# Kernel tuning notes

Hardware: AMD Instinct MI355X
Metric: run time of the kernel (lower is better)

## Reference

```python
import jax, jax.numpy as jnp
import numpy as np

LAMBDA = 0.01  # sparsity_threshold
SCALE = 0.02
NUM_BLOCKS = 4


def setup_inputs() -> dict:
    key = jax.random.key(0)
    k1, k2, k3, k4, k5 = jax.random.split(key, 5)
    B, N, C = 8, 4096, 512
    bs = C // NUM_BLOCKS
    return {
        "x": jax.random.normal(k1, (B, N, C), dtype=jnp.float32),
        "w1": jax.random.normal(k2, (2, NUM_BLOCKS, bs, bs), dtype=jnp.float32) * SCALE,
        "w2": jax.random.normal(k3, (2, NUM_BLOCKS, bs, bs), dtype=jnp.float32) * SCALE,
        "b1": jax.random.normal(k4, (2, NUM_BLOCKS, bs), dtype=jnp.float32) * SCALE,
        "b2": jax.random.normal(k5, (2, NUM_BLOCKS, bs), dtype=jnp.float32) * SCALE,
        "H": 64,
        "W": 64,
    }


def _softshrink(v):
    return jnp.where(v > LAMBDA, v - LAMBDA, jnp.where(v < -LAMBDA, v + LAMBDA, jnp.zeros((), v.dtype)))


def reference(x, w1, w2, b1, b2, H, W):
    B, N, C = x.shape
    bs = C // NUM_BLOCKS
    xb = x.reshape(B, N, NUM_BLOCKS, bs)
    # FFT over (token, block) axes, ortho norm — faithful to torch fft2(dim=(1,2))
    xf = jnp.fft.fft2(xb, axes=(1, 2), norm="ortho")
    re, im = jnp.real(xf), jnp.imag(xf)

    mul = lambda a, w: jnp.einsum("tnbd,bdk->tnbk", a, w)  # block-diagonal matmul

    r1 = jax.nn.relu(mul(re, w1[0]) - mul(im, w1[1]) + b1[0])
    i1 = jax.nn.relu(mul(re, w1[1]) + mul(im, w1[0]) + b1[1])
    r2 = mul(r1, w2[0]) - mul(i1, w2[1]) + b2[0]
    i2 = mul(r1, w2[1]) + mul(i1, w2[0]) + b2[1]

    z = _softshrink(r2) + 1j * _softshrink(i2)
    out = jnp.real(jnp.fft.ifft2(z, axes=(1, 2), norm="ortho"))  # .to(float32) keeps real part
    return out.reshape(B, N, C).astype(jnp.float32)
```

## Files before the change

kernel.cpp:

```cpp
#include <hip/hip_runtime.h>
#include <math.h>

#define TWO_PI 6.283185307179586f

typedef __attribute__((ext_vector_type(8))) short bf16x8;
typedef __attribute__((ext_vector_type(4))) short bf16x4;
typedef __attribute__((ext_vector_type(4))) float f32x4;
typedef __attribute__((ext_vector_type(4))) _Float16 h16x4;
typedef __attribute__((ext_vector_type(8))) _Float16 h16x8;

__device__ __forceinline__ short f2bf(float f) {
    unsigned u = __float_as_uint(f);
    unsigned r = (u + 0x7FFFu + ((u >> 16) & 1u)) >> 16;
    return (short)r;
}
__device__ __forceinline__ float bf2f(short s) {
    return __uint_as_float(((unsigned)(unsigned short)s) << 16);
}

__device__ __forceinline__ int dr4(int s) {
    return ((s & 3) << 4) | (s & 12) | ((s >> 4) & 3);
}

__device__ __forceinline__ void cmulw(float& xr, float& xi, float wr, float wi) {
    const float tr = xr * wr - xi * wi;
    xi = xr * wi + xi * wr;
    xr = tr;
}

__device__ __forceinline__ f32x4 ld4bf(const char* Z, int off) {
    const bf16x4 v = *(const bf16x4*)(Z + off);
    f32x4 r;
    r[0] = bf2f(v[0]); r[1] = bf2f(v[1]); r[2] = bf2f(v[2]); r[3] = bf2f(v[3]);
    return r;
}
__device__ __forceinline__ void st4bf(char* Z, int off, f32x4 a) {
    bf16x4 v;
    v[0] = f2bf(a[0]); v[1] = f2bf(a[1]); v[2] = f2bf(a[2]); v[3] = f2bf(a[3]);
    *(bf16x4*)(Z + off) = v;
}

__device__ __forceinline__ int swzoff(int r, int cb) {
    return r * 256 + (cb ^ ((r & 7) << 4));
}

__device__ __forceinline__ void dif_stage_bf(char* Z, const float* wtr, const float* wti,
                                             int cb, int h, int s) {
    const int q  = 16 >> (2 * s);
    const int tw = 1 << (2 * s);
    const int j = h & (q - 1);
    const int g = (s == 0) ? 0 : (h >> (4 - 2 * s));
    const int i0 = g * (q << 2) + j;
    const int i1 = i0 + q, i2 = i1 + q, i3 = i2 + q;
    const int o0 = swzoff(i0, cb), o1 = swzoff(i1, cb);
    const int o2 = swzoff(i2, cb), o3 = swzoff(i3, cb);
    const f32x4 a0r = ld4bf(Z, o0), a0i = ld4bf(Z + 16384, o0);
    const f32x4 a1r = ld4bf(Z, o1), a1i = ld4bf(Z + 16384, o1);
    const f32x4 a2r = ld4bf(Z, o2), a2i = ld4bf(Z + 16384, o2);
    const f32x4 a3r = ld4bf(Z, o3), a3i = ld4bf(Z + 16384, o3);
    const int m = j * tw;
    const float w1r = wtr[m],     w1i = wti[m];
    const float w2r = wtr[2 * m], w2i = wti[2 * m];
    const float w3r = wtr[3 * m], w3i = wti[3 * m];
    f32x4 O0r, O0i, O1r, O1i, O2r, O2i, O3r, O3i;
#pragma unroll
    for (int e = 0; e < 4; ++e) {
        const float t0r = a0r[e] + a2r[e], t0i = a0i[e] + a2i[e];
        const float t2r = a0r[e] - a2r[e], t2i = a0i[e] - a2i[e];
        const float t1r = a1r[e] + a3r[e], t1i = a1i[e] + a3i[e];
        const float dr  = a1r[e] - a3r[e], di  = a1i[e] - a3i[e];
        const float t3r = di, t3i = -dr;
        O0r[e] = t0r + t1r;  O0i[e] = t0i + t1i;
        float y1r = t2r + t3r, y1i = t2i + t3i;
        float y2r = t0r - t1r, y2i = t0i - t1i;
        float y3r = t2r - t3r, y3i = t2i - t3i;
        if (m) {
            cmulw(y1r, y1i, w1r, w1i);
            cmulw(y2r, y2i, w2r, w2i);
            cmulw(y3r, y3i, w3r, w3i);
        }
        O1r[e] = y1r; O1i[e] = y1i;
        O2r[e] = y2r; O2i[e] = y2i;
        O3r[e] = y3r; O3i[e] = y3i;
    }
    st4bf(Z, o0, O0r);  st4bf(Z + 16384, o0, O0i);
    st4bf(Z, o1, O1r);  st4bf(Z + 16384, o1, O1i);
    st4bf(Z, o2, O2r);  st4bf(Z + 16384, o2, O2i);
    st4bf(Z, o3, O3r);  st4bf(Z + 16384, o3, O3i);
}

__device__ __forceinline__ void dit_stage_bf(char* Z, const float* wtr, const float* wti,
                                             int cb, int h, int s) {
    const int q  = 16 >> (2 * s);
    const int tw = 1 << (2 * s);
    const int j = h & (q - 1);
    const int g = (s == 0) ? 0 : (h >> (4 - 2 * s));
    const int i0 = g * (q << 2) + j;
    const int i1 = i0 + q, i2 = i1 + q, i3 = i2 + q;
    const int o0 = swzoff(i0, cb), o1 = swzoff(i1, cb);
    const int o2 = swzoff(i2, cb), o3 = swzoff(i3, cb);
    const f32x4 a0r = ld4bf(Z, o0), a0i = ld4bf(Z + 16384, o0);
    const f32x4 a1r = ld4bf(Z, o1), a1i = ld4bf(Z + 16384, o1);
    const f32x4 a2r = ld4bf(Z, o2), a2i = ld4bf(Z + 16384, o2);
    const f32x4 a3r = ld4bf(Z, o3), a3i = ld4bf(Z + 16384, o3);
    const int m = j * tw;
    const float w1r = wtr[m],     w1i = -wti[m];
    const float w2r = wtr[2 * m], w2i = -wti[2 * m];
    const float w3r = wtr[3 * m], w3i = -wti[3 * m];
    f32x4 O0r, O0i, O1r, O1i, O2r, O2i, O3r, O3i;
#pragma unroll
    for (int e = 0; e < 4; ++e) {
        float b1r = a1r[e], b1i = a1i[e];
        float b2r = a2r[e], b2i = a2i[e];
        float b3r = a3r[e], b3i = a3i[e];
        if (m) {
            cmulw(b1r, b1i, w1r, w1i);
            cmulw(b2r, b2i, w2r, w2i);
            cmulw(b3r, b3i, w3r, w3i);
        }
        const float u0r = a0r[e] + b2r, u0i = a0i[e] + b2i;
        const float u1r = a0r[e] - b2r, u1i = a0i[e] - b2i;
        const float u2r = b1r + b3r,    u2i = b1i + b3i;
        const float dr  = b1r - b3r,    di  = b1i - b3i;
        const float u3r = -di, u3i = dr;
        O0r[e] = u0r + u2r; O0i[e] = u0i + u2i;
        O1r[e] = u1r + u3r; O1i[e] = u1i + u3i;
        O2r[e] = u0r - u2r; O2i[e] = u0i - u2i;
        O3r[e] = u1r - u3r; O3i[e] = u1i - u3i;
    }
    st4bf(Z, o0, O0r);  st4bf(Z + 16384, o0, O0i);
    st4bf(Z, o1, O1r);  st4bf(Z + 16384, o1, O1i);
    st4bf(Z, o2, O2r);  st4bf(Z + 16384, o2, O2i);
    st4bf(Z, o3, O3r);  st4bf(Z + 16384, o3, O3i);
}

__device__ __forceinline__ void stage_ztile(const short* __restrict__ zre,
                                            const short* __restrict__ zim,
                                            char* Zbuf, int b, int dg, int ct,
                                            int wave, int lane) {
#pragma unroll
    for (int it = 0; it < 4; ++it) {
        const int q = wave * 256 + it * 64 + lane;
        const int p = q >> 10;
        const int r = q & 1023;
        const int slot = r >> 4;
        const int c = r & 15;
        const int c_log = c ^ (slot & 7);
        const int blk = c_log >> 2, cj = c_log & 3;
        const short* src = p ? zim : zre;
        const size_t g = ((size_t)(b * 4096 + dg * 64 + slot) * 512)
                       + (size_t)(blk * 128 + ct * 32 + cj * 8);
        unsigned* lp = (unsigned*)(Zbuf + (wave * 4096 + it * 1024));
        __builtin_amdgcn_global_load_lds((const unsigned*)(src + g), lp, 16, 0, 0);
    }
}

#define DECODE_BCT() \
    const int b  = blockIdx.x >> 8; \
    const int dg = (blockIdx.x >> 2) & 63; \
    const int ct = blockIdx.x & 3;

#define GADDR(slot, blk, f4) \
    (((size_t)(b * 4096 + (slot)) * 512) + (size_t)((blk) * 128 + ct * 32 + (f4) * 4))

#define SETUP_TABLE48() \
    if (tid < 48) { \
        float s_, c_; \
        sincosf(TWO_PI * (float)tid / 64.0f, &s_, &c_); \
        wre[tid] = c_; wim[tid] = -s_; \
    }

template<int W>
__device__ __forceinline__ void fft64_dif4v(_Float16 (*Lre)[W], _Float16 (*Lim)[W],
                                            const float* wtr, const float* wti,
                                            int c4, int h) {
#pragma unroll
    for (int s = 0; s < 3; ++s) {
        const int q  = 16 >> (2 * s);
        const int tw = 1 << (2 * s);
        __syncthreads();
        const int j = h & (q - 1);
        const int g = (s == 0) ? 0 : (h >> (4 - 2 * s));
        const int i0 = g * (q << 2) + j;
        const int i1 = i0 + q, i2 = i1 + q, i3 = i2 + q;
        const h16x4 A0r = *(const h16x4*)&Lre[i0][c4], A0i = *(const h16x4*)&Lim[i0][c4];
        const h16x4 A1r = *(const h16x4*)&Lre[i1][c4], A1i = *(const h16x4*)&Lim[i1][c4];
        const h16x4 A2r = *(const h16x4*)&Lre[i2][c4], A2i = *(const h16x4*)&Lim[i2][c4];
        const h16x4 A3r = *(const h16x4*)&Lre[i3][c4], A3i = *(const h16x4*)&Lim[i3][c4];
        const int m = j * tw;
        const float w1r = wtr[m],     w1i = wti[m];
        const float w2r = wtr[2 * m], w2i = wti[2 * m];
        const float w3r = wtr[3 * m], w3i = wti[3 * m];
        h16x4 O0r, O0i, O1r, O1i, O2r, O2i, O3r, O3i;
#pragma unroll
        for (int e = 0; e < 4; ++e) {
            const float a0r = (float)A0r[e], a0i = (float)A0i[e];
            const float a1r = (float)A1r[e], a1i = (float)A1i[e];
            const float a2r = (float)A2r[e], a2i = (float)A2i[e];
            const float a3r = (float)A3r[e], a3i = (float)A3i[e];
            const float t0r = a0r + a2r, t0i = a0i + a2i;
            const float t2r = a0r - a2r, t2i = a0i - a2i;
            const float t1r = a1r + a3r, t1i = a1i + a3i;
            const float dr  = a1r - a3r, di  = a1i - a3i;
            const float t3r = di, t3i = -dr;
            O0r[e] = (_Float16)(t0r + t1r);  O0i[e] = (_Float16)(t0i + t1i);
            float y1r = t2r + t3r, y1i = t2i + t3i;
            float y2r = t0r - t1r, y2i = t0i - t1i;
            float y3r = t2r - t3r, y3i = t2i - t3i;
            if (m) {
                cmulw(y1r, y1i, w1r, w1i);
                cmulw(y2r, y2i, w2r, w2i);
                cmulw(y3r, y3i, w3r, w3i);
            }
            O1r[e] = (_Float16)y1r; O1i[e] = (_Float16)y1i;
            O2r[e] = (_Float16)y2r; O2i[e] = (_Float16)y2i;
            O3r[e] = (_Float16)y3r; O3i[e] = (_Float16)y3i;
        }
        *(h16x4*)&Lre[i0][c4] = O0r;  *(h16x4*)&Lim[i0][c4] = O0i;
        *(h16x4*)&Lre[i1][c4] = O1r;  *(h16x4*)&Lim[i1][c4] = O1i;
        *(h16x4*)&Lre[i2][c4] = O2r;  *(h16x4*)&Lim[i2][c4] = O2i;
        *(h16x4*)&Lre[i3][c4] = O3r;  *(h16x4*)&Lim[i3][c4] = O3i;
    }
    __syncthreads();
}

template<int W>
__device__ __forceinline__ void fft64_dit4v(_Float16 (*Lre)[W], _Float16 (*Lim)[W],
                                            const float* wtr, const float* wti,
                                            int c4, int h) {
#pragma unroll
    for (int s = 2; s >= 0; --s) {
        const int q  = 16 >> (2 * s);
        const int tw = 1 << (2 * s);
        __syncthreads();
        const int j = h & (q - 1);
        const int g = (s == 0) ? 0 : (h >> (4 - 2 * s));
        const int i0 = g * (q << 2) + j;
        const int i1 = i0 + q, i2 = i1 + q, i3 = i2 + q;
        const h16x4 A0r = *(const h16x4*)&Lre[i0][c4], A0i = *(const h16x4*)&Lim[i0][c4];
        const h16x4 A1r = *(const h16x4*)&Lre[i1][c4], A1i = *(const h16x4*)&Lim[i1][c4];
        const h16x4 A2r = *(const h16x4*)&Lre[i2][c4], A2i = *(const h16x4*)&Lim[i2][c4];
        const h16x4 A3r = *(const h16x4*)&Lre[i3][c4], A3i = *(const h16x4*)&Lim[i3][c4];
        const int m = j * tw;
        const float w1r = wtr[m],     w1i = -wti[m];
        const float w2r = wtr[2 * m], w2i = -wti[2 * m];
        const float w3r = wtr[3 * m], w3i = -wti[3 * m];
        h16x4 O0r, O0i, O1r, O1i, O2r, O2i, O3r, O3i;
#pragma unroll
        for (int e = 0; e < 4; ++e) {
            float b1r = (float)A1r[e], b1i = (float)A1i[e];
            float b2r = (float)A2r[e], b2i = (float)A2i[e];
            float b3r = (float)A3r[e], b3i = (float)A3i[e];
            if (m) {
                cmulw(b1r, b1i, w1r, w1i);
                cmulw(b2r, b2i, w2r, w2i);
                cmulw(b3r, b3i, w3r, w3i);
            }
            const float a0r = (float)A0r[e], a0i = (float)A0i[e];
            const float u0r = a0r + b2r, u0i = a0i + b2i;
            const float u1r = a0r - b2r, u1i = a0i - b2i;
            const float u2r = b1r + b3r, u2i = b1i + b3i;
            const float dr  = b1r - b3r, di  = b1i - b3i;
            const float u3r = -di, u3i = dr;
            O0r[e] = (_Float16)(u0r + u2r); O0i[e] = (_Float16)(u0i + u2i);
            O1r[e] = (_Float16)(u1r + u3r); O1i[e] = (_Float16)(u1i + u3i);
            O2r[e] = (_Float16)(u0r - u2r); O2i[e] = (_Float16)(u0i - u2i);
            O3r[e] = (_Float16)(u1r - u3r); O3i[e] = (_Float16)(u1i - u3i);
        }
        *(h16x4*)&Lre[i0][c4] = O0r;  *(h16x4*)&Lim[i0][c4] = O0i;
        *(h16x4*)&Lre[i1][c4] = O1r;  *(h16x4*)&Lim[i1][c4] = O1i;
        *(h16x4*)&Lre[i2][c4] = O2r;  *(h16x4*)&Lim[i2][c4] = O2i;
        *(h16x4*)&Lre[i3][c4] = O3r;  *(h16x4*)&Lim[i3][c4] = O3i;
    }
    __syncthreads();
}

extern "C" __global__ void __launch_bounds__(512)
fft_fwd_a(const float* __restrict__ x, short* __restrict__ zre, short* __restrict__ zim) {
    __shared__ __align__(16) _Float16 Lre[64][136];
    __shared__ __align__(16) _Float16 Lim[64][136];
    __shared__ float wre[48], wim[48];
    __shared__ float twr[64], twi[64];
    const int tid = threadIdx.x;
    SETUP_TABLE48();
    DECODE_BCT();
    if (tid >= 64 && tid < 128) {
        const int s1 = tid - 64;
        float sn, cs;
        sincosf(-(TWO_PI / 4096.0f) * (float)(dg * dr4(s1)), &sn, &cs);
        twr[s1] = cs; twi[s1] = sn;
    }
    for (int idx = tid; idx < 2048; idx += 512) {
        const int n1 = idx >> 5, q = idx & 31, blk = q >> 3, f4 = q & 7;
        const int cl = blk * 32 + f4 * 4;
        const float4 v = *(const float4*)(x + GADDR(n1 * 64 + dg, blk, f4));
        h16x4 hv, hz;
        hv[0] = (_Float16)v.x; hv[1] = (_Float16)v.y;
        hv[2] = (_Float16)v.z; hv[3] = (_Float16)v.w;
        hz[0] = (_Float16)0.f; hz[1] = (_Float16)0.f;
        hz[2] = (_Float16)0.f; hz[3] = (_Float16)0.f;
        *(h16x4*)&Lre[n1][cl] = hv;
        *(h16x4*)&Lim[n1][cl] = hz;
    }
    fft64_dif4v<136>(Lre, Lim, wre, wim, (tid & 31) * 4, tid >> 5);
    {
        const int s1 = tid >> 3, f4 = tid & 7;
        const float cs = twr[s1], sn = twi[s1];
        f32x4 r[4], m[4];
#pragma unroll
        for (int blk = 0; blk < 4; ++blk) {
            const int cl = blk * 32 + f4 * 4;
            const h16x4 hr = *(const h16x4*)&Lre[s1][cl];
            const h16x4 hi = *(const h16x4*)&Lim[s1][cl];
#pragma unroll
            for (int e = 0; e < 4; ++e) {
                const float vr = (float)hr[e], vi = (float)hi[e];
                r[blk][e] = vr * cs - vi * sn;
                m[blk][e] = vr * sn + vi * cs;
            }
        }
        const float sc = 1.0f / 128.0f;
        f32x4 yr[4], ym[4];
#pragma unroll
        for (int e = 0; e < 4; ++e) {
            const float r0 = r[0][e], r1 = r[1][e], r2 = r[2][e], r3 = r[3][e];
            const float m0 = m[0][e], m1 = m[1][e], m2 = m[2][e], m3 = m[3][e];
            yr[0][e] = (r0 + r1 + r2 + r3) * sc;  ym[0][e] = (m0 + m1 + m2 + m3) * sc;
            yr[1][e] = (r0 + m1 - r2 - m3) * sc;  ym[1][e] = (m0 - r1 - m2 + r3) * sc;
            yr[2][e] = (r0 - r1 + r2 - r3) * sc;  ym[2][e] = (m0 - m1 + m2 - m3) * sc;
            yr[3][e] = (r0 - m1 - r2 + m3) * sc;  ym[3][e] = (m0 + r1 - m2 - r3) * sc;
        }
#pragma unroll
        for (int blk = 0; blk < 4; ++blk) {
            bf16x4 pr, pi;
#pragma unroll
            for (int e = 0; e < 4; ++e) {
                pr[e] = f2bf(yr[blk][e]);
                pi[e] = f2bf(ym[blk][e]);
            }
            const size_t g = GADDR(s1 * 64 + dg, blk, f4);
            *(bf16x4*)(zre + g) = pr;
            *(bf16x4*)(zim + g) = pi;
        }
    }
}

extern "C" __global__ void __launch_bounds__(512)
fft_fwd_b(short* __restrict__ zre, short* __restrict__ zim) {
    __shared__ __align__(16) char Zs[32768];
    __shared__ float wre[48], wim[48];
    const int tid = threadIdx.x;
    SETUP_TABLE48();
    const int bh = blockIdx.x >> 8;
    const int dg = (blockIdx.x >> 2) & 63;
    const int ct = blockIdx.x & 3;
    const int wave = tid >> 6, lane = tid & 63;
    const int cb = (tid & 31) * 8;
    const int h  = tid >> 5;

    stage_ztile(zre, zim, Zs, bh * 2, dg, ct, wave, lane);

    for (int t = 0; t < 2; ++t) {
        __syncthreads();
        dif_stage_bf(Zs, wre, wim, cb, h, 0);
        __syncthreads();
        dif_stage_bf(Zs, wre, wim, cb, h, 1);
        __syncthreads();
        dif_stage_bf(Zs, wre, wim, cb, h, 2);
        __syncthreads();
        bf16x8 vout[4];
#pragma unroll
        for (int kq = 0; kq < 4; ++kq) {
            const int q = wave * 256 + kq * 64 + lane;
            vout[kq] = *(const bf16x8*)(Zs + q * 16);
        }
        __syncthreads();
        if (t + 1 < 2)
            stage_ztile(zre, zim, Zs, bh * 2 + t + 1, dg, ct, wave, lane);
        const int b = bh * 2 + t;
#pragma unroll
        for (int kq = 0; kq < 4; ++kq) {
            const int q = wave * 256 + kq * 64 + lane;
            const int p = q >> 10;
            const int r2 = q & 1023;
            const int slot = r2 >> 4;
            const int c = r2 & 15;
            const int c_log = c ^ (slot & 7);
            const int blk = c_log >> 2, cj = c_log & 3;
            short* dst = p ? zim : zre;
            const size_t g = ((size_t)(b * 4096 + dg * 64 + slot) * 512)
                           + (size_t)(blk * 128 + ct * 32 + cj * 8);
            *(bf16x8*)(dst + g) = vout[kq];
        }
    }
}

extern "C" __global__ void __launch_bounds__(512)
fft_inv_a(short* __restrict__ zre, short* __restrict__ zim) {
    __shared__ __align__(16) char Zs[32768];
    __shared__ float wre[48], wim[48];
    __shared__ float twr[64], twi[64];
    const int tid = threadIdx.x;
    SETUP_TABLE48();
    const int bh = blockIdx.x >> 8;
    const int dg = (blockIdx.x >> 2) & 63;
    const int ct = blockIdx.x & 3;
    if (tid >= 64 && tid < 128) {
        const int n2 = tid - 64;
        float sn, cs;
        sincosf((TWO_PI / 4096.0f) * (float)(n2 * dr4(dg)), &sn, &cs);
        twr[n2] = cs; twi[n2] = sn;
    }
    const int wave = tid >> 6, lane = tid & 63;
    const int cb = (tid & 31) * 8;
    const int h  = tid >> 5;

    stage_ztile(zre, zim, Zs, bh * 2, dg, ct, wave, lane);

    for (int t = 0; t < 2; ++t) {
        __syncthreads();
        dit_stage_bf(Zs, wre, wim, cb, h, 2);
        __syncthreads();
        dit_stage_bf(Zs, wre, wim, cb, h, 1);
        __syncthreads();
        dit_stage_bf(Zs, wre, wim, cb, h, 0);
        __syncthreads();
        bf16x8 pr[2], pi[2];
#pragma unroll
        for (int k = 0; k < 2; ++k) {
            const int idx = tid + k * 512;
            const int slot = idx >> 4;
            const int c = idx & 15;
            const bf16x8 vr = *(const bf16x8*)(Zs + slot * 256 + c * 16);
            const bf16x8 vi = *(const bf16x8*)(Zs + 16384 + slot * 256 + c * 16);
            const float cs = twr[slot], sn = twi[slot];
#pragma unroll
            for (int i = 0; i < 8; ++i) {
                const float ar = bf2f(vr[i]), ai = bf2f(vi[i]);
                pr[k][i] = f2bf(ar * cs - ai * sn);
                pi[k][i] = f2bf(ar * sn + ai * cs);
            }
        }
        __syncthreads();
        if (t + 1 < 2)
            stage_ztile(zre, zim, Zs, bh * 2 + t + 1, dg, ct, wave, lane);
        const int b = bh * 2 + t;
#pragma unroll
        for (int k = 0; k < 2; ++k) {
            const int idx = tid + k * 512;
            const int slot = idx >> 4;
            const int c = idx & 15;
            const int c_log = c ^ (slot & 7);
            const int blk = c_log >> 2, cj = c_log & 3;
            const size_t g = ((size_t)(b * 4096 + dg * 64 + slot) * 512)
                           + (size_t)(blk * 128 + ct * 32 + cj * 8);
            *(bf16x8*)(zre + g) = pr[k];
            *(bf16x8*)(zim + g) = pi[k];
        }
    }
}

extern "C" __global__ void __launch_bounds__(512)
fft_inv_b(const short* __restrict__ zre, const short* __restrict__ zim,
          float* __restrict__ out) {
    __shared__ __align__(16) _Float16 Lre[64][136];
    __shared__ __align__(16) _Float16 Lim[64][136];
    __shared__ float wre[48], wim[48];
    const int tid = threadIdx.x;
    SETUP_TABLE48();
    DECODE_BCT();
    {
        const int s1 = tid >> 3, f4 = tid & 7;
        f32x4 r[4], m[4];
#pragma unroll
        for (int blk = 0; blk < 4; ++blk) {
            const size_t g = GADDR(s1 * 64 + dg, blk, f4);
            const bf16x4 vr = *(const bf16x4*)(zre + g);
            const bf16x4 vi = *(const bf16x4*)(zim + g);
#pragma unroll
            for (int e = 0; e < 4; ++e) {
                r[blk][e] = bf2f(vr[e]);
                m[blk][e] = bf2f(vi[e]);
            }
        }
        const float sc = 1.0f / 128.0f;
        f32x4 yr[4], ym[4];
#pragma unroll
        for (int e = 0; e < 4; ++e) {
            const float r0 = r[0][e], r1 = r[1][e], r2 = r[2][e], r3 = r[3][e];
            const float m0 = m[0][e], m1 = m[1][e], m2 = m[2][e], m3 = m[3][e];
            yr[0][e] = (r0 + r1 + r2 + r3) * sc;  ym[0][e] = (m0 + m1 + m2 + m3) * sc;
            yr[1][e] = (r0 - m1 - r2 + m3) * sc;  ym[1][e] = (m0 + r1 - m2 - r3) * sc;
            yr[2][e] = (r0 - r1 + r2 - r3) * sc;  ym[2][e] = (m0 - m1 + m2 - m3) * sc;
            yr[3][e] = (r0 + m1 - r2 - m3) * sc;  ym[3][e] = (m0 - r1 - m2 + r3) * sc;
        }
#pragma unroll
        for (int blk = 0; blk < 4; ++blk) {
            const int cl = blk * 32 + f4 * 4;
            h16x4 hr, hi;
#pragma unroll
            for (int e = 0; e < 4; ++e) {
                hr[e] = (_Float16)yr[blk][e];
                hi[e] = (_Float16)ym[blk][e];
            }
            *(h16x4*)&Lre[s1][cl] = hr;
            *(h16x4*)&Lim[s1][cl] = hi;
        }
    }
    fft64_dit4v<136>(Lre, Lim, wre, wim, (tid & 31) * 4, tid >> 5);
    for (int idx = tid; idx < 2048; idx += 512) {
        const int n1 = idx >> 5, q = idx & 31, blk = q >> 3, f4 = q & 7;
        const int cl = blk * 32 + f4 * 4;
        const h16x4 hr = *(const h16x4*)&Lre[n1][cl];
        float4 o;
        o.x = (float)hr[0]; o.y = (float)hr[1];
        o.z = (float)hr[2]; o.w = (float)hr[3];
        *(float4*)(out + GADDR(n1 * 64 + dg, blk, f4)) = o;
    }
}

extern "C" __global__ void __launch_bounds__(256)
wprep(const float* __restrict__ w1, const float* __restrict__ w2,
      short* __restrict__ wb) {
    const int i4  = blockIdx.x * 256 + threadIdx.x;
    const int k0  = (i4 & 63) * 4;
    const int n   = (i4 >> 6) & 255;
    const int blk = (i4 >> 14) & 3;
    const int L   = i4 >> 16;
    const float* w = L ? w2 : w1;
    bf16x4 pv;
#pragma unroll
    for (int j = 0; j < 4; ++j) {
        const int k = k0 + j;
        float v;
        if (k < 128) {
            v = (n < 128) ? w[blk * 16384 + k * 128 + n]
                          : w[65536 + blk * 16384 + k * 128 + (n - 128)];
        } else {
            v = (n < 128) ? -w[65536 + blk * 16384 + (k - 128) * 128 + n]
                          :  w[blk * 16384 + (k - 128) * 128 + (n - 128)];
        }
        pv[j] = f2bf(v);
    }
    *(bf16x4*)(wb + (size_t)i4 * 4) = pv;
}

#define MITER 4

__device__ __forceinline__ void stage_tile(const short* __restrict__ zre,
                                           const short* __restrict__ zim,
                                           char* Abuf, int rowbase, int blk,
                                           int wave, int lane) {
#pragma unroll
    for (int it = 0; it < 4; ++it) {
        const int chunk = wave * 256 + it * 64 + lane;
        const int row   = chunk >> 5;
        const unsigned kbyte = ((unsigned)((chunk & 31) << 4)) ^ ((unsigned)((row & 7) << 4));
        const int k0 = (int)(kbyte >> 1);
        const short* src = (k0 < 128) ? zre : zim;
        const size_t g = (size_t)(rowbase + row) * 512 + blk * 128 + (k0 & 127);
        unsigned* lp = (unsigned*)(Abuf + (wave * 4096 + it * 1024));
        __builtin_amdgcn_global_load_lds((const unsigned*)(src + g), lp, 16, 0, 0);
    }
}

template<int LAYER>
__global__ void __launch_bounds__(512)
mlp_mfma(short* __restrict__ zre, short* __restrict__ zim,
         const short* __restrict__ wb, const float* __restrict__ bias) {
    __shared__ __align__(16) char As[2][64 * 256 * 2];

    const int blk  = blockIdx.y;
    const int tid  = threadIdx.x;
    const int wave = tid >> 6;
    const int lane = tid & 63;
    const int lrow = lane & 15;
    const int lk   = lane >> 4;

    bf16x8 Bf[2][8];
#pragma unroll
    for (int nt = 0; nt < 2; ++nt) {
        const int n = wave * 32 + nt * 16 + lrow;
#pragma unroll
        for (int ks = 0; ks < 8; ++ks) {
            Bf[nt][ks] = *(const bf16x8*)(wb + ((size_t)(blk * 256 + n) * 256 + ks * 32 + lk * 8));
        }
    }

    float bv[2];
#pragma unroll
    for (int nt = 0; nt < 2; ++nt) {
        const int n = wave * 32 + nt * 16 + lrow;
        bv[nt] = (n < 128) ? bias[blk * 128 + n] : bias[512 + blk * 128 + (n - 128)];
    }

    stage_tile(zre, zim, As[0], blockIdx.x * MITER * 64, blk, wave, lane);

    for (int t = 0; t < MITER; ++t) {
        __syncthreads();

        if (t + 1 < MITER)
            stage_tile(zre, zim, As[(t + 1) & 1],
                       (blockIdx.x * MITER + t + 1) * 64, blk, wave, lane);

        const char* Ab = As[t & 1];
        const int rowbase = (blockIdx.x * MITER + t) * 64;

        f32x4 acc[4][2];
#pragma unroll
        for (int mt = 0; mt < 4; ++mt)
#pragma unroll
            for (int nt = 0; nt < 2; ++nt)
                acc[mt][nt] = (f32x4){0.f, 0.f, 0.f, 0.f};

#pragma unroll
        for (int ks = 0; ks < 8; ++ks) {
            bf16x8 af[4];
#pragma unroll
            for (int mt = 0; mt < 4; ++mt) {
                const int row = mt * 16 + lrow;
                const int k0  = ks * 32 + lk * 8;
                const unsigned byteoff =
                    ((unsigned)(row * 512 + k0 * 2)) ^ ((unsigned)((row & 7) << 4));
                af[mt] = *(const bf16x8*)(Ab + byteoff);
            }
#pragma unroll
            for (int mt = 0; mt < 4; ++mt)
#pragma unroll
                for (int nt = 0; nt < 2; ++nt)
                    acc[mt][nt] = __builtin_amdgcn_mfma_f32_16x16x32_bf16(
                        af[mt], Bf[nt][ks], acc[mt][nt], 0, 0, 0);
        }

#pragma unroll
        for (int nt = 0; nt < 2; ++nt) {
            const int n = wave * 32 + nt * 16 + lrow;
            short* dst = (n < 128) ? zre : zim;
            const int col = blk * 128 + (n & 127);
#pragma unroll
            for (int mt = 0; mt < 4; ++mt) {
#pragma unroll
                for (int r = 0; r < 4; ++r) {
                    const int row = rowbase + mt * 16 + lk * 4 + r;
                    float v = acc[mt][nt][r] + bv[nt];
                    if (LAYER == 1) {
                        v = fmaxf(v, 0.0f);
                    } else {
                        v = (v > 0.01f) ? v - 0.01f : ((v < -0.01f) ? v + 0.01f : 0.0f);
                    }
                    dst[(size_t)row * 512 + col] = f2bf(v);
                }
            }
        }
    }
}

extern "C" void kernel_launch(void* const* d_in, const int* in_sizes, int n_in,
                              void* d_out, int out_size, void* d_ws, size_t ws_size,
                              hipStream_t stream) {
    const float* x  = (const float*)d_in[0];
    const float* w1 = (const float*)d_in[1];
    const float* w2 = (const float*)d_in[2];
    const float* b1 = (const float*)d_in[3];
    const float* b2 = (const float*)d_in[4];

    float* out = (float*)d_out;
    short* zre = (short*)d_ws;
    short* zim = zre + 16777216;
    short* wb  = (short*)d_out;
    const size_t WB_L = 4ull * 256 * 256;

    wprep<<<512, 256, 0, stream>>>(w1, w2, wb);

    fft_fwd_a<<<2048, 512, 0, stream>>>(x, zre, zim);
    fft_fwd_b<<<1024, 512, 0, stream>>>(zre, zim);

    mlp_mfma<1><<<dim3(32768 / (64 * MITER), 4), 512, 0, stream>>>(zre, zim, wb, b1);
    mlp_mfma<2><<<dim3(32768 / (64 * MITER), 4), 512, 0, stream>>>(zre, zim, wb + WB_L, b2);

    fft_inv_a<<<1024, 512, 0, stream>>>(zre, zim);
    fft_inv_b<<<2048, 512, 0, stream>>>(zre, zim, out);
}
```

Measured before the change: 222.5 us.

## Fuse second FFT stage passes into the MLP matmul kernels

Removes the separate fft_fwd_b and fft_inv_a kernels. Their radix-4 64-point passes now run on the shared-memory A tile inside the layer-1 MLP kernel before the matmul. In the layer-2 kernel, the inverse passes plus the twiddle multiply run on the tile after the softshrink epilogue. This saves two full global read/write round trips of the bf16 spectrum and two launches. In exchange the MLP kernels take extra barriers, per-element sincos calls and FFT arithmetic that delay the MFMA work and the prefetch issue.

```diff
diff --git a/kernel.cpp b/kernel.cpp
--- a/kernel.cpp
+++ b/kernel.cpp
@@ -40,24 +40,38 @@
     *(bf16x4*)(Z + off) = v;
 }
 
-__device__ __forceinline__ int swzoff(int r, int cb) {
-    return r * 256 + (cb ^ ((r & 7) << 4));
-}
-
-__device__ __forceinline__ void dif_stage_bf(char* Z, const float* wtr, const float* wti,
-                                             int cb, int h, int s) {
+#define DECODE_BCT() \
+    const int b  = blockIdx.x >> 8; \
+    const int dg = (blockIdx.x >> 2) & 63; \
+    const int ct = blockIdx.x & 3;
+
+#define GADDR(slot, blk, f4) \
+    (((size_t)(b * 4096 + (slot)) * 512) + (size_t)((blk) * 128 + ct * 32 + (f4) * 4))
+
+#define SETUP_TABLE48() \
+    if (tid < 48) { \
+        float s_, c_; \
+        sincosf(TWO_PI * (float)tid / 64.0f, &s_, &c_); \
+        wre[tid] = c_; wim[tid] = -s_; \
+    }
+
+__device__ __forceinline__ void dif_stage_A(char* Z, const float* wtr, const float* wti,
+                                            int cg, int h, int s) {
     const int q  = 16 >> (2 * s);
     const int tw = 1 << (2 * s);
     const int j = h & (q - 1);
     const int g = (s == 0) ? 0 : (h >> (4 - 2 * s));
     const int i0 = g * (q << 2) + j;
     const int i1 = i0 + q, i2 = i1 + q, i3 = i2 + q;
-    const int o0 = swzoff(i0, cb), o1 = swzoff(i1, cb);
-    const int o2 = swzoff(i2, cb), o3 = swzoff(i3, cb);
-    const f32x4 a0r = ld4bf(Z, o0), a0i = ld4bf(Z + 16384, o0);
-    const f32x4 a1r = ld4bf(Z, o1), a1i = ld4bf(Z + 16384, o1);
-    const f32x4 a2r = ld4bf(Z, o2), a2i = ld4bf(Z + 16384, o2);
-    const f32x4 a3r = ld4bf(Z, o3), a3i = ld4bf(Z + 16384, o3);
+    const int cbR = cg * 8, cbI = cbR + 256;
+    const int oR0 = i0 * 512 + (cbR ^ ((i0 & 7) << 4)), oI0 = i0 * 512 + (cbI ^ ((i0 & 7) << 4));
+    const int oR1 = i1 * 512 + (cbR ^ ((i1 & 7) << 4)), oI1 = i1 * 512 + (cbI ^ ((i1 & 7) << 4));
+    const int oR2 = i2 * 512 + (cbR ^ ((i2 & 7) << 4)), oI2 = i2 * 512 + (cbI ^ ((i2 & 7) << 4));
+    const int oR3 = i3 * 512 + (cbR ^ ((i3 & 7) << 4)), oI3 = i3 * 512 + (cbI ^ ((i3 & 7) << 4));
+    const f32x4 a0r = ld4bf(Z, oR0), a0i = ld4bf(Z, oI0);
+    const f32x4 a1r = ld4bf(Z, oR1), a1i = ld4bf(Z, oI1);
+    const f32x4 a2r = ld4bf(Z, oR2), a2i = ld4bf(Z, oI2);
+    const f32x4 a3r = ld4bf(Z, oR3), a3i = ld4bf(Z, oI3);
     const int m = j * tw;
     const float w1r = wtr[m],     w1i = wti[m];
     const float w2r = wtr[2 * m], w2i = wti[2 * m];
@@ -83,26 +97,29 @@
         O2r[e] = y2r; O2i[e] = y2i;
         O3r[e] = y3r; O3i[e] = y3i;
     }
-    st4bf(Z, o0, O0r);  st4bf(Z + 16384, o0, O0i);
-    st4bf(Z, o1, O1r);  st4bf(Z + 16384, o1, O1i);
-    st4bf(Z, o2, O2r);  st4bf(Z + 16384, o2, O2i);
-    st4bf(Z, o3, O3r);  st4bf(Z + 16384, o3, O3i);
-}
-
-__device__ __forceinline__ void dit_stage_bf(char* Z, const float* wtr, const float* wti,
-                                             int cb, int h, int s) {
+    st4bf(Z, oR0, O0r);  st4bf(Z, oI0, O0i);
+    st4bf(Z, oR1, O1r);  st4bf(Z, oI1, O1i);
+    st4bf(Z, oR2, O2r);  st4bf(Z, oI2, O2i);
+    st4bf(Z, oR3, O3r);  st4bf(Z, oI3, O3i);
+}
+
+__device__ __forceinline__ void dit_stage_A(char* Z, const float* wtr, const float* wti,
+                                            int cg, int h, int s) {
     const int q  = 16 >> (2 * s);
     const int tw = 1 << (2 * s);
     const int j = h & (q - 1);
     const int g = (s == 0) ? 0 : (h >> (4 - 2 * s));
     const int i0 = g * (q << 2) + j;
     const int i1 = i0 + q, i2 = i1 + q, i3 = i2 + q;
-    const int o0 = swzoff(i0, cb), o1 = swzoff(i1, cb);
-    const int o2 = swzoff(i2, cb), o3 = swzoff(i3, cb);
-    const f32x4 a0r = ld4bf(Z, o0), a0i = ld4bf(Z + 16384, o0);
-    const f32x4 a1r = ld4bf(Z, o1), a1i = ld4bf(Z + 16384, o1);
-    const f32x4 a2r = ld4bf(Z, o2), a2i = ld4bf(Z + 16384, o2);
-    const f32x4 a3r = ld4bf(Z, o3), a3i = ld4bf(Z + 16384, o3);
+    const int cbR = cg * 8, cbI = cbR + 256;
+    const int oR0 = i0 * 512 + (cbR ^ ((i0 & 7) << 4)), oI0 = i0 * 512 + (cbI ^ ((i0 & 7) << 4));
+    const int oR1 = i1 * 512 + (cbR ^ ((i1 & 7) << 4)), oI1 = i1 * 512 + (cbI ^ ((i1 & 7) << 4));
+    const int oR2 = i2 * 512 + (cbR ^ ((i2 & 7) << 4)), oI2 = i2 * 512 + (cbI ^ ((i2 & 7) << 4));
+    const int oR3 = i3 * 512 + (cbR ^ ((i3 & 7) << 4)), oI3 = i3 * 512 + (cbI ^ ((i3 & 7) << 4));
+    const f32x4 a0r = ld4bf(Z, oR0), a0i = ld4bf(Z, oI0);
+    const f32x4 a1r = ld4bf(Z, oR1), a1i = ld4bf(Z, oI1);
+    const f32x4 a2r = ld4bf(Z, oR2), a2i = ld4bf(Z, oI2);
+    const f32x4 a3r = ld4bf(Z, oR3), a3i = ld4bf(Z, oI3);
     const int m = j * tw;
     const float w1r = wtr[m],     w1i = -wti[m];
     const float w2r = wtr[2 * m], w2i = -wti[2 * m];
@@ -128,47 +145,11 @@
         O2r[e] = u0r - u2r; O2i[e] = u0i - u2i;
         O3r[e] = u1r - u3r; O3i[e] = u1i - u3i;
     }
-    st4bf(Z, o0, O0r);  st4bf(Z + 16384, o0, O0i);
-    st4bf(Z, o1, O1r);  st4bf(Z + 16384, o1, O1i);
-    st4bf(Z, o2, O2r);  st4bf(Z + 16384, o2, O2i);
-    st4bf(Z, o3, O3r);  st4bf(Z + 16384, o3, O3i);
-}
-
-__device__ __forceinline__ void stage_ztile(const short* __restrict__ zre,
-                                            const short* __restrict__ zim,
-                                            char* Zbuf, int b, int dg, int ct,
-                                            int wave, int lane) {
-#pragma unroll
-    for (int it = 0; it < 4; ++it) {
-        const int q = wave * 256 + it * 64 + lane;
-        const int p = q >> 10;
-        const int r = q & 1023;
-        const int slot = r >> 4;
-        const int c = r & 15;
-        const int c_log = c ^ (slot & 7);
-        const int blk = c_log >> 2, cj = c_log & 3;
-        const short* src = p ? zim : zre;
-        const size_t g = ((size_t)(b * 4096 + dg * 64 + slot) * 512)
-                       + (size_t)(blk * 128 + ct * 32 + cj * 8);
-        unsigned* lp = (unsigned*)(Zbuf + (wave * 4096 + it * 1024));
-        __builtin_amdgcn_global_load_lds((const unsigned*)(src + g), lp, 16, 0, 0);
-    }
-}
-
-#define DECODE_BCT() \
-    const int b  = blockIdx.x >> 8; \
-    const int dg = (blockIdx.x >> 2) & 63; \
-    const int ct = blockIdx.x & 3;
-
-#define GADDR(slot, blk, f4) \
-    (((size_t)(b * 4096 + (slot)) * 512) + (size_t)((blk) * 128 + ct * 32 + (f4) * 4))
-
-#define SETUP_TABLE48() \
-    if (tid < 48) { \
-        float s_, c_; \
-        sincosf(TWO_PI * (float)tid / 64.0f, &s_, &c_); \
-        wre[tid] = c_; wim[tid] = -s_; \
-    }
+    st4bf(Z, oR0, O0r);  st4bf(Z, oI0, O0i);
+    st4bf(Z, oR1, O1r);  st4bf(Z, oI1, O1i);
+    st4bf(Z, oR2, O2r);  st4bf(Z, oI2, O2i);
+    st4bf(Z, oR3, O3r);  st4bf(Z, oI3, O3i);
+}
 
 template<int W>
 __device__ __forceinline__ void fft64_dif4v(_Float16 (*Lre)[W], _Float16 (*Lim)[W],
@@ -346,121 +327,6 @@
 }
 
 extern "C" __global__ void __launch_bounds__(512)
-fft_fwd_b(short* __restrict__ zre, short* __restrict__ zim) {
-    __shared__ __align__(16) char Zs[32768];
-    __shared__ float wre[48], wim[48];
-    const int tid = threadIdx.x;
-    SETUP_TABLE48();
-    const int bh = blockIdx.x >> 8;
-    const int dg = (blockIdx.x >> 2) & 63;
-    const int ct = blockIdx.x & 3;
-    const int wave = tid >> 6, lane = tid & 63;
-    const int cb = (tid & 31) * 8;
-    const int h  = tid >> 5;
-
-    stage_ztile(zre, zim, Zs, bh * 2, dg, ct, wave, lane);
-
-    for (int t = 0; t < 2; ++t) {
-        __syncthreads();
-        dif_stage_bf(Zs, wre, wim, cb, h, 0);
-        __syncthreads();
-        dif_stage_bf(Zs, wre, wim, cb, h, 1);
-        __syncthreads();
-        dif_stage_bf(Zs, wre, wim, cb, h, 2);
-        __syncthreads();
-        bf16x8 vout[4];
-#pragma unroll
-        for (int kq = 0; kq < 4; ++kq) {
-            const int q = wave * 256 + kq * 64 + lane;
-            vout[kq] = *(const bf16x8*)(Zs + q * 16);
-        }
-        __syncthreads();
-        if (t + 1 < 2)
-            stage_ztile(zre, zim, Zs, bh * 2 + t + 1, dg, ct, wave, lane);
-        const int b = bh * 2 + t;
-#pragma unroll
-        for (int kq = 0; kq < 4; ++kq) {
-            const int q = wave * 256 + kq * 64 + lane;
-            const int p = q >> 10;
-            const int r2 = q & 1023;
-            const int slot = r2 >> 4;
-            const int c = r2 & 15;
-            const int c_log = c ^ (slot & 7);
-            const int blk = c_log >> 2, cj = c_log & 3;
-            short* dst = p ? zim : zre;
-            const size_t g = ((size_t)(b * 4096 + dg * 64 + slot) * 512)
-                           + (size_t)(blk * 128 + ct * 32 + cj * 8);
-            *(bf16x8*)(dst + g) = vout[kq];
-        }
-    }
-}
-
-extern "C" __global__ void __launch_bounds__(512)
-fft_inv_a(short* __restrict__ zre, short* __restrict__ zim) {
-    __shared__ __align__(16) char Zs[32768];
-    __shared__ float wre[48], wim[48];
-    __shared__ float twr[64], twi[64];
-    const int tid = threadIdx.x;
-    SETUP_TABLE48();
-    const int bh = blockIdx.x >> 8;
-    const int dg = (blockIdx.x >> 2) & 63;
-    const int ct = blockIdx.x & 3;
-    if (tid >= 64 && tid < 128) {
-        const int n2 = tid - 64;
-        float sn, cs;
-        sincosf((TWO_PI / 4096.0f) * (float)(n2 * dr4(dg)), &sn, &cs);
-        twr[n2] = cs; twi[n2] = sn;
-    }
-    const int wave = tid >> 6, lane = tid & 63;
-    const int cb = (tid & 31) * 8;
-    const int h  = tid >> 5;
-
-    stage_ztile(zre, zim, Zs, bh * 2, dg, ct, wave, lane);
-
-    for (int t = 0; t < 2; ++t) {
-        __syncthreads();
-        dit_stage_bf(Zs, wre, wim, cb, h, 2);
-        __syncthreads();
-        dit_stage_bf(Zs, wre, wim, cb, h, 1);
-        __syncthreads();
-        dit_stage_bf(Zs, wre, wim, cb, h, 0);
-        __syncthreads();
-        bf16x8 pr[2], pi[2];
-#pragma unroll
-        for (int k = 0; k < 2; ++k) {
-            const int idx = tid + k * 512;
-            const int slot = idx >> 4;
-            const int c = idx & 15;
-            const bf16x8 vr = *(const bf16x8*)(Zs + slot * 256 + c * 16);
-            const bf16x8 vi = *(const bf16x8*)(Zs + 16384 + slot * 256 + c * 16);
-            const float cs = twr[slot], sn = twi[slot];
-#pragma unroll
-            for (int i = 0; i < 8; ++i) {
-                const float ar = bf2f(vr[i]), ai = bf2f(vi[i]);
-                pr[k][i] = f2bf(ar * cs - ai * sn);
-                pi[k][i] = f2bf(ar * sn + ai * cs);
-            }
-        }
-        __syncthreads();
-        if (t + 1 < 2)
-            stage_ztile(zre, zim, Zs, bh * 2 + t + 1, dg, ct, wave, lane);
-        const int b = bh * 2 + t;
-#pragma unroll
-        for (int k = 0; k < 2; ++k) {
-            const int idx = tid + k * 512;
-            const int slot = idx >> 4;
-            const int c = idx & 15;
-            const int c_log = c ^ (slot & 7);
-            const int blk = c_log >> 2, cj = c_log & 3;
-            const size_t g = ((size_t)(b * 4096 + dg * 64 + slot) * 512)
-                           + (size_t)(blk * 128 + ct * 32 + cj * 8);
-            *(bf16x8*)(zre + g) = pr[k];
-            *(bf16x8*)(zim + g) = pi[k];
-        }
-    }
-}
-
-extern "C" __global__ void __launch_bounds__(512)
 fft_inv_b(const short* __restrict__ zre, const short* __restrict__ zim,
           float* __restrict__ out) {
     __shared__ __align__(16) _Float16 Lre[64][136];
@@ -566,9 +432,10 @@
 
 template<int LAYER>
 __global__ void __launch_bounds__(512)
-mlp_mfma(short* __restrict__ zre, short* __restrict__ zim,
-         const short* __restrict__ wb, const float* __restrict__ bias) {
+mlp_fused(short* __restrict__ zre, short* __restrict__ zim,
+          const short* __restrict__ wb, const float* __restrict__ bias) {
     __shared__ __align__(16) char As[2][64 * 256 * 2];
+    __shared__ float wre[48], wim[48];
 
     const int blk  = blockIdx.y;
     const int tid  = threadIdx.x;
@@ -576,6 +443,9 @@
     const int lane = tid & 63;
     const int lrow = lane & 15;
     const int lk   = lane >> 4;
+    const int cg   = tid & 31;
+    const int fh   = tid >> 5;
+    SETUP_TABLE48();
 
     bf16x8 Bf[2][8];
 #pragma unroll
@@ -599,12 +469,21 @@
     for (int t = 0; t < MITER; ++t) {
         __syncthreads();
 
+        char* Ab = As[t & 1];
+        const int rowbase = (blockIdx.x * MITER + t) * 64;
+
+        if (LAYER == 1) {
+            dif_stage_A(Ab, wre, wim, cg, fh, 0);
+            __syncthreads();
+            dif_stage_A(Ab, wre, wim, cg, fh, 1);
+            __syncthreads();
+            dif_stage_A(Ab, wre, wim, cg, fh, 2);
+            __syncthreads();
+        }
+
         if (t + 1 < MITER)
             stage_tile(zre, zim, As[(t + 1) & 1],
                        (blockIdx.x * MITER + t + 1) * 64, blk, wave, lane);
-
-        const char* Ab = As[t & 1];
-        const int rowbase = (blockIdx.x * MITER + t) * 64;
 
         f32x4 acc[4][2];
 #pragma unroll
@@ -632,24 +511,70 @@
                         af[mt], Bf[nt][ks], acc[mt][nt], 0, 0, 0);
         }
 
-#pragma unroll
-        for (int nt = 0; nt < 2; ++nt) {
-            const int n = wave * 32 + nt * 16 + lrow;
-            short* dst = (n < 128) ? zre : zim;
-            const int col = blk * 128 + (n & 127);
-#pragma unroll
-            for (int mt = 0; mt < 4; ++mt) {
-#pragma unroll
-                for (int r = 0; r < 4; ++r) {
-                    const int row = rowbase + mt * 16 + lk * 4 + r;
-                    float v = acc[mt][nt][r] + bv[nt];
-                    if (LAYER == 1) {
-                        v = fmaxf(v, 0.0f);
-                    } else {
+        if (LAYER == 1) {
+#pragma unroll
+            for (int nt = 0; nt < 2; ++nt) {
+                const int n = wave * 32 + nt * 16 + lrow;
+                short* dst = (n < 128) ? zre : zim;
+                const int col = blk * 128 + (n & 127);
+#pragma unroll
+                for (int mt = 0; mt < 4; ++mt) {
+#pragma unroll
+                    for (int r = 0; r < 4; ++r) {
+                        const int row = rowbase + mt * 16 + lk * 4 + r;
+                        const float v = fmaxf(acc[mt][nt][r] + bv[nt], 0.0f);
+                        dst[(size_t)row * 512 + col] = f2bf(v);
+                    }
+                }
+            }
+        } else {
+            __syncthreads();
+#pragma unroll
+            for (int nt = 0; nt < 2; ++nt) {
+                const int n = wave * 32 + nt * 16 + lrow;
+                const int cb = n * 2;
+#pragma unroll
+                for (int mt = 0; mt < 4; ++mt) {
+#pragma unroll
+                    for (int r = 0; r < 4; ++r) {
+                        const int row = mt * 16 + lk * 4 + r;
+                        float v = acc[mt][nt][r] + bv[nt];
                         v = (v > 0.01f) ? v - 0.01f : ((v < -0.01f) ? v + 0.01f : 0.0f);
+                        *(short*)(Ab + row * 512 + (cb ^ ((row & 7) << 4))) = f2bf(v);
                     }
-                    dst[(size_t)row * 512 + col] = f2bf(v);
                 }
+            }
+            __syncthreads();
+            dit_stage_A(Ab, wre, wim, cg, fh, 2);
+            __syncthreads();
+            dit_stage_A(Ab, wre, wim, cg, fh, 1);
+            __syncthreads();
+            dit_stage_A(Ab, wre, wim, cg, fh, 0);
+            __syncthreads();
+            const int s1 = rowbase >> 6;
+            const int k1 = dr4(s1 & 63);
+#pragma unroll
+            for (int kk = 0; kk < 4; ++kk) {
+                const int idx = tid + kk * 512;
+                const int row = idx >> 5;
+                const int q = idx & 31;
+                const int p = q >> 4;
+                const int c = q & 15;
+                const int cbyte = p * 256 + c * 16;
+                bf16x8 v = *(const bf16x8*)(Ab + row * 512 + (cbyte ^ ((row & 7) << 4)));
+                float sn, cs;
+                sincosf((TWO_PI / 4096.0f) * (float)(row * k1), &sn, &cs);
+                const int cbyte2 = (p ? 0 : 256) + c * 16;
+                bf16x8 v2 = *(const bf16x8*)(Ab + row * 512 + (cbyte2 ^ ((row & 7) << 4)));
+                bf16x8 o;
+#pragma unroll
+                for (int e = 0; e < 8; ++e) {
+                    const float ar = p ? bf2f(v2[e]) : bf2f(v[e]);
+                    const float ai = p ? bf2f(v[e]) : bf2f(v2[e]);
+                    o[e] = p ? f2bf(ar * sn + ai * cs) : f2bf(ar * cs - ai * sn);
+                }
+                short* dst = p ? zim : zre;
+                *(bf16x8*)(dst + (size_t)(rowbase + row) * 512 + blk * 128 + c * 8) = o;
             }
         }
     }
@@ -673,11 +598,9 @@
     wprep<<<512, 256, 0, stream>>>(w1, w2, wb);
 
     fft_fwd_a<<<2048, 512, 0, stream>>>(x, zre, zim);
-    fft_fwd_b<<<1024, 512, 0, stream>>>(zre, zim);
-
-    mlp_mfma<1><<<dim3(32768 / (64 * MITER), 4), 512, 0, stream>>>(zre, zim, wb, b1);
-    mlp_mfma<2><<<dim3(32768 / (64 * MITER), 4), 512, 0, stream>>>(zre, zim, wb + WB_L, b2);
-
-    fft_inv_a<<<1024, 512, 0, stream>>>(zre, zim);
+
+    mlp_fused<1><<<dim3(32768 / (64 * MITER), 4), 512, 0, stream>>>(zre, zim, wb, b1);
+    mlp_fused<2><<<dim3(32768 / (64 * MITER), 4), 512, 0, stream>>>(zre, zim, wb + WB_L, b2);
+
     fft_inv_b<<<2048, 512, 0, stream>>>(zre, zim, out);
 }
```

Measured after the change: 213.5 us. 1.04x faster.
